# Performance work log

Measured on AMD Instinct MI355X. Metric: run time of the kernel, lower is better.

The kernel has to match this reference:

```python
import jax, jax.numpy as jnp
import numpy as np

# Module hyperparameters (from init_kwargs)
KH, KW = 3, 3          # kernel_size (must be 3x3: code hardcodes center tap 4 and 9 search positions)
SH, SW = 1, 1          # stride
PH, PW = 4, 4          # padding
DH, DW = 4, 4          # dilation
SD = DH // 2           # search_dilation


def setup_inputs() -> dict:
    key = jax.random.key(0)
    # positive depth values in meters-like range
    depth = jax.random.uniform(key, (4, 1, 480, 640), dtype=jnp.float32) * 10.0
    return {"depth": depth}


def _offset_search(depth):
    b, _, h, w = depth.shape
    outH = (h + 2 * PH - DH * (KH - 1) - 1) // SH + 1
    outW = (w + 2 * PW - DW * (KW - 1) - 1) // SW + 1
    d = depth[:, 0]  # [b, h, w]

    # --- first unfold: 3x3 window, dilation=SD, padding=SD, stride=1 ---
    # 9 zero-padded shifted copies of the depth map (the search samples)
    dp = jnp.pad(d, ((0, 0), (SD, SD), (SD, SD)))
    S = jnp.stack([dp[:, SD * r: SD * r + h, SD * c: SD * c + w]
                   for r in range(3) for c in range(3)], axis=1)  # [b, 9, h, w]

    # --- second unfold: kernel 3x3, dilation=(DH,DW), padding=(PH,PW), stride=(SH,SW) ---
    Sp = jnp.pad(S, ((0, 0), (0, 0), (PH, PH), (PW, PW)))
    rspan = SH * (outH - 1) + 1
    cspan = SW * (outW - 1) + 1
    taps = [Sp[:, :, DH * r: DH * r + rspan: SH, DW * c: DW * c + cspan: SW]
            for r in range(KH) for c in range(KW)]
    sample = jnp.stack(taps, axis=2)  # [b, 9(search), 9(kernel), outH, outW]

    # --- center tap (index 4) of unfold(depth) ---
    dpp = jnp.pad(d, ((0, 0), (PH, PH), (PW, PW)))
    center = dpp[:, DH: DH + rspan: SH, DW: DW + cspan: SW]  # [b, outH, outW]

    sample = jnp.abs(sample - center[:, None, None])

    # mask invalid search positions with +inf for border kernel taps 1,3,5,7
    inf = jnp.float32(jnp.inf)
    row_idx = jnp.array([0, 1, 2, 6, 7, 8])
    col_idx = jnp.array([0, 2, 3, 5, 6, 8])
    sample = sample.at[:, col_idx, 1].set(inf)
    sample = sample.at[:, row_idx, 3].set(inf)
    sample = sample.at[:, row_idx, 5].set(inf)
    sample = sample.at[:, col_idx, 7].set(inf)

    # argmin over the 9 search positions (first occurrence, like torch.min)
    idx = jnp.argmin(sample, axis=1)          # [b, 9, outH, outW]
    off_h = (idx // KH - 1) * SD
    off_w = (idx % KW - 1) * SD
    return jnp.concatenate([off_h, off_w], axis=1).astype(jnp.int32)  # [b, 18, outH, outW]


def reference(depth):
    return _offset_search(depth)
```

## Files before the change

kernel.cpp:

```cpp
#include <hip/hip_runtime.h>


#define BATCH 4
#define IH 480
#define IW 640

__global__ __launch_bounds__(256) void depth_offset_kernel(
    const float* __restrict__ d, int* __restrict__ out) {
  int idx = blockIdx.x * blockDim.x + threadIdx.x;
  if (idx >= BATCH * IH * IW) return;
  int ox = idx % IW;
  int t = idx / IW;
  int oy = t % IH;
  int b = t / IH;

  const float* __restrict__ db = d + (size_t)b * (IH * IW);
  float center = db[oy * IW + ox];

  const size_t plane = (size_t)IH * IW;
  int* __restrict__ outb = out + (size_t)b * 18 * plane;
  size_t pix = (size_t)oy * IW + ox;

  bool interior = (oy >= 6) & (oy <= IH - 7) & (ox >= 6) & (ox <= IW - 7);

  if (interior) {
    float nb[7][7];
    const float* p = db + (oy - 6) * IW + (ox - 6);
#pragma unroll
    for (int i = 0; i < 7; ++i) {
#pragma unroll
      for (int jj = 0; jj < 7; ++jj) {
        nb[i][jj] = p[(2 * i) * IW + 2 * jj];
      }
    }

#pragma unroll
    for (int j = 0; j < 9; ++j) {
      const int jr = j / 3, jc = j % 3;
      float best = __builtin_huge_valf();
      int bk = 0;
#pragma unroll
      for (int k = 0; k < 9; ++k) {
        const int kr = k / 3, kc = k % 3;
        bool allowed = true;
        if (j == 1 || j == 7) allowed = (kc == 1);
        if (j == 3 || j == 5) allowed = (kr == 1);
        if (!allowed) continue;

        float diff = fabsf(nb[2 * jr + kr][2 * jc + kc] - center);
        if (diff < best) {
          best = diff;
          bk = k;
        }
      }
      __builtin_nontemporal_store((bk / 3 - 1) * 2, &outb[(size_t)j * plane + pix]);
      __builtin_nontemporal_store((bk % 3 - 1) * 2, &outb[(size_t)(9 + j) * plane + pix]);
    }
  } else {
    float nb[7][7];
#pragma unroll
    for (int i = 0; i < 7; ++i) {
      int y = oy + 2 * i - 6;
      bool yok = ((unsigned)y < (unsigned)IH);
#pragma unroll
      for (int jj = 0; jj < 7; ++jj) {
        int x = ox + 2 * jj - 6;
        float v = 0.0f;
        if (yok && ((unsigned)x < (unsigned)IW)) v = db[y * IW + x];
        nb[i][jj] = v;
      }
    }

#pragma unroll
    for (int j = 0; j < 9; ++j) {
      const int jr = j / 3, jc = j % 3;
      int Y = oy + 4 * (jr - 1);
      int X = ox + 4 * (jc - 1);
      bool jok = ((unsigned)Y < (unsigned)IH) && ((unsigned)X < (unsigned)IW);

      float best = __builtin_huge_valf();
      int bk = 0;
#pragma unroll
      for (int k = 0; k < 9; ++k) {
        const int kr = k / 3, kc = k % 3;
        bool allowed = true;
        if (j == 1 || j == 7) allowed = (kc == 1);
        if (j == 3 || j == 5) allowed = (kr == 1);
        if (!allowed) continue;

        float v = jok ? nb[2 * jr + kr][2 * jc + kc] : 0.0f;
        float diff = fabsf(v - center);
        if (diff < best) {
          best = diff;
          bk = k;
        }
      }
      __builtin_nontemporal_store((bk / 3 - 1) * 2, &outb[(size_t)j * plane + pix]);
      __builtin_nontemporal_store((bk % 3 - 1) * 2, &outb[(size_t)(9 + j) * plane + pix]);
    }
  }
}

extern "C" void kernel_launch(void* const* d_in, const int* in_sizes, int n_in,
                              void* d_out, int out_size, void* d_ws, size_t ws_size,
                              hipStream_t stream) {
  const float* depth = (const float*)d_in[0];
  int* out = (int*)d_out;
  const int total = BATCH * IH * IW;
  const int block = 256;
  const int grid = (total + block - 1) / block;
  depth_offset_kernel<<<grid, block, 0, stream>>>(depth, out);
}
```

Before: 109.1 us.

## Compute four adjacent pixels per thread with vectorized row loads and stores

Each thread now handles four consecutive output pixels. It loads seven 20-float row segments with 128-bit vector loads, shares them across the four pixels, and writes each of the 18 output planes with one 128-bit nontemporal store. The goal is fewer scalar global loads and wider store transactions on a kernel that writes a large output. In exchange each thread uses more registers (a 7x20 array), the grid has fewer threads, and the border path now loops over four pixels per thread.

```diff
diff --git a/kernel.cpp b/kernel.cpp
--- a/kernel.cpp
+++ b/kernel.cpp
@@ -4,99 +4,141 @@
 #define BATCH 4
 #define IH 480
 #define IW 640
+#define W4 (IW / 4)
+
+typedef int iv4 __attribute__((ext_vector_type(4)));
+typedef float fv4 __attribute__((ext_vector_type(4)));
 
 __global__ __launch_bounds__(256) void depth_offset_kernel(
     const float* __restrict__ d, int* __restrict__ out) {
-  int idx = blockIdx.x * blockDim.x + threadIdx.x;
-  if (idx >= BATCH * IH * IW) return;
-  int ox = idx % IW;
-  int t = idx / IW;
+  int tid = blockIdx.x * blockDim.x + threadIdx.x;
+  if (tid >= BATCH * IH * W4) return;
+  int ox4 = tid % W4;
+  int ox = ox4 * 4;
+  int t = tid / W4;
   int oy = t % IH;
   int b = t / IH;
 
   const float* __restrict__ db = d + (size_t)b * (IH * IW);
-  float center = db[oy * IW + ox];
-
   const size_t plane = (size_t)IH * IW;
   int* __restrict__ outb = out + (size_t)b * 18 * plane;
   size_t pix = (size_t)oy * IW + ox;
 
-  bool interior = (oy >= 6) & (oy <= IH - 7) & (ox >= 6) & (ox <= IW - 7);
+  bool interior = (oy >= 6) & (oy <= IH - 7) & (ox >= 8) & (ox <= IW - 12);
 
   if (interior) {
-    float nb[7][7];
-    const float* p = db + (oy - 6) * IW + (ox - 6);
+    float cen[4];
+    {
+      const fv4 c4 = *reinterpret_cast<const fv4*>(db + pix);
+      cen[0] = c4.x; cen[1] = c4.y; cen[2] = c4.z; cen[3] = c4.w;
+    }
+    const float* p = db + (size_t)(oy - 6) * IW + (ox - 8);
+
+    float rows[7][20];
+    auto load_row = [&](int i) {
 #pragma unroll
-    for (int i = 0; i < 7; ++i) {
+      for (int v = 0; v < 5; ++v) {
+        const fv4 r =
+            *reinterpret_cast<const fv4*>(p + (size_t)(2 * i) * IW + 4 * v);
+        rows[i][4 * v + 0] = r.x;
+        rows[i][4 * v + 1] = r.y;
+        rows[i][4 * v + 2] = r.z;
+        rows[i][4 * v + 3] = r.w;
+      }
+    };
+
+    load_row(0);
+    load_row(1);
+    load_row(2);
+
 #pragma unroll
-      for (int jj = 0; jj < 7; ++jj) {
-        nb[i][jj] = p[(2 * i) * IW + 2 * jj];
+    for (int jr = 0; jr < 3; ++jr) {
+      if (jr == 1) { load_row(3); load_row(4); }
+      if (jr == 2) { load_row(5); load_row(6); }
+#pragma unroll
+      for (int jc = 0; jc < 3; ++jc) {
+        const int j = jr * 3 + jc;
+        int bks[4];
+#pragma unroll
+        for (int q = 0; q < 4; ++q) {
+          float best = __builtin_huge_valf();
+          int bk = 0;
+#pragma unroll
+          for (int k = 0; k < 9; ++k) {
+            const int kr = k / 3, kc = k % 3;
+            bool allowed = true;
+            if (j == 1 || j == 7) allowed = (kc == 1);
+            if (j == 3 || j == 5) allowed = (kr == 1);
+            if (!allowed) continue;
+
+            float diff =
+                fabsf(rows[2 * jr + kr][q + 2 + 2 * (2 * jc + kc)] - cen[q]);
+            if (diff < best) {
+              best = diff;
+              bk = k;
+            }
+          }
+          bks[q] = bk;
+        }
+        iv4 oh, ow;
+        oh.x = (bks[0] / 3 - 1) * 2; oh.y = (bks[1] / 3 - 1) * 2;
+        oh.z = (bks[2] / 3 - 1) * 2; oh.w = (bks[3] / 3 - 1) * 2;
+        ow.x = (bks[0] % 3 - 1) * 2; ow.y = (bks[1] % 3 - 1) * 2;
+        ow.z = (bks[2] % 3 - 1) * 2; ow.w = (bks[3] % 3 - 1) * 2;
+        __builtin_nontemporal_store(
+            oh, reinterpret_cast<iv4*>(outb + (size_t)j * plane + pix));
+        __builtin_nontemporal_store(
+            ow, reinterpret_cast<iv4*>(outb + (size_t)(9 + j) * plane + pix));
       }
     }
+  } else {
+#pragma unroll
+    for (int q = 0; q < 4; ++q) {
+      const int x0 = ox + q;
+      const float center = db[oy * IW + x0];
+      float nb[7][7];
+#pragma unroll
+      for (int i = 0; i < 7; ++i) {
+        int y = oy + 2 * i - 6;
+        bool yok = ((unsigned)y < (unsigned)IH);
+#pragma unroll
+        for (int jj = 0; jj < 7; ++jj) {
+          int x = x0 + 2 * jj - 6;
+          float v = 0.0f;
+          if (yok && ((unsigned)x < (unsigned)IW)) v = db[y * IW + x];
+          nb[i][jj] = v;
+        }
+      }
 
 #pragma unroll
-    for (int j = 0; j < 9; ++j) {
-      const int jr = j / 3, jc = j % 3;
-      float best = __builtin_huge_valf();
-      int bk = 0;
+      for (int j = 0; j < 9; ++j) {
+        const int jr = j / 3, jc = j % 3;
+        int Y = oy + 4 * (jr - 1);
+        int X = x0 + 4 * (jc - 1);
+        bool jok = ((unsigned)Y < (unsigned)IH) && ((unsigned)X < (unsigned)IW);
+
+        float best = __builtin_huge_valf();
+        int bk = 0;
 #pragma unroll
-      for (int k = 0; k < 9; ++k) {
-        const int kr = k / 3, kc = k % 3;
-        bool allowed = true;
-        if (j == 1 || j == 7) allowed = (kc == 1);
-        if (j == 3 || j == 5) allowed = (kr == 1);
-        if (!allowed) continue;
+        for (int k = 0; k < 9; ++k) {
+          const int kr = k / 3, kc = k % 3;
+          bool allowed = true;
+          if (j == 1 || j == 7) allowed = (kc == 1);
+          if (j == 3 || j == 5) allowed = (kr == 1);
+          if (!allowed) continue;
 
-        float diff = fabsf(nb[2 * jr + kr][2 * jc + kc] - center);
-        if (diff < best) {
-          best = diff;
-          bk = k;
+          float v = jok ? nb[2 * jr + kr][2 * jc + kc] : 0.0f;
+          float diff = fabsf(v - center);
+          if (diff < best) {
+            best = diff;
+            bk = k;
+          }
         }
+        __builtin_nontemporal_store(
+            (bk / 3 - 1) * 2, &outb[(size_t)j * plane + pix + q]);
+        __builtin_nontemporal_store(
+            (bk % 3 - 1) * 2, &outb[(size_t)(9 + j) * plane + pix + q]);
       }
-      __builtin_nontemporal_store((bk / 3 - 1) * 2, &outb[(size_t)j * plane + pix]);
-      __builtin_nontemporal_store((bk % 3 - 1) * 2, &outb[(size_t)(9 + j) * plane + pix]);
-    }
-  } else {
-    float nb[7][7];
-#pragma unroll
-    for (int i = 0; i < 7; ++i) {
-      int y = oy + 2 * i - 6;
-      bool yok = ((unsigned)y < (unsigned)IH);
-#pragma unroll
-      for (int jj = 0; jj < 7; ++jj) {
-        int x = ox + 2 * jj - 6;
-        float v = 0.0f;
-        if (yok && ((unsigned)x < (unsigned)IW)) v = db[y * IW + x];
-        nb[i][jj] = v;
-      }
-    }
-
-#pragma unroll
-    for (int j = 0; j < 9; ++j) {
-      const int jr = j / 3, jc = j % 3;
-      int Y = oy + 4 * (jr - 1);
-      int X = ox + 4 * (jc - 1);
-      bool jok = ((unsigned)Y < (unsigned)IH) && ((unsigned)X < (unsigned)IW);
-
-      float best = __builtin_huge_valf();
-      int bk = 0;
-#pragma unroll
-      for (int k = 0; k < 9; ++k) {
-        const int kr = k / 3, kc = k % 3;
-        bool allowed = true;
-        if (j == 1 || j == 7) allowed = (kc == 1);
-        if (j == 3 || j == 5) allowed = (kr == 1);
-        if (!allowed) continue;
-
-        float v = jok ? nb[2 * jr + kr][2 * jc + kc] : 0.0f;
-        float diff = fabsf(v - center);
-        if (diff < best) {
-          best = diff;
-          bk = k;
-        }
-      }
-      __builtin_nontemporal_store((bk / 3 - 1) * 2, &outb[(size_t)j * plane + pix]);
-      __builtin_nontemporal_store((bk % 3 - 1) * 2, &outb[(size_t)(9 + j) * plane + pix]);
     }
   }
 }
@@ -106,7 +148,7 @@
                               hipStream_t stream) {
   const float* depth = (const float*)d_in[0];
   int* out = (int*)d_out;
-  const int total = BATCH * IH * IW;
+  const int total = BATCH * IH * W4;
   const int block = 256;
   const int grid = (total + block - 1) / block;
   depth_offset_kernel<<<grid, block, 0, stream>>>(depth, out);
```

Result: slower. 130.8 us (+19.9%).
